# Performance work log

Hardware: AMD Instinct MI355X
Metric: run time of the kernel (lower is better)

## Reference

```python
import jax, jax.numpy as jnp
import numpy as np
import math

B, LQ, LK = 2, 2048, 2048
DIM = 1024
H = 16
DH = DIM // H


def setup_inputs() -> dict:
    key = jax.random.key(0)
    ks = jax.random.split(key, 12)
    s = 1.0 / math.sqrt(DIM)
    return {
        "query": jax.random.normal(ks[0], (B, LQ, DIM), jnp.float32),
        "key": jax.random.normal(ks[1], (B, LK, DIM), jnp.float32),
        "value": jax.random.normal(ks[2], (B, LK, DIM), jnp.float32),
        "mask": jnp.zeros((B, LQ, LK), dtype=bool),
        "Wq": jax.random.normal(ks[3], (DIM, DIM), jnp.float32) * s,
        "bq": jax.random.normal(ks[4], (DIM,), jnp.float32) * s,
        "Wk": jax.random.normal(ks[5], (DIM, DIM), jnp.float32) * s,
        "bk": jax.random.normal(ks[6], (DIM,), jnp.float32) * s,
        "Wv": jax.random.normal(ks[7], (DIM, DIM), jnp.float32) * s,
        "bv": jax.random.normal(ks[8], (DIM,), jnp.float32) * s,
        "Wo": jax.random.normal(ks[9], (DIM, DIM), jnp.float32) * s,
        "bo": jax.random.normal(ks[10], (DIM,), jnp.float32) * s,
    }


def reference(query, key, value, mask, Wq, bq, Wk, bk, Wv, bv, Wo, bo):
    b = query.shape[0]

    def shape(x):  # (b, l, dim) -> (b, h, l, dh)
        return x.reshape(b, -1, H, DH).transpose(0, 2, 1, 3)

    q = shape(query @ Wq.T + bq)
    k = shape(key @ Wk.T + bk)
    v = shape(value @ Wv.T + bv)

    q = q / math.sqrt(DH)
    # (b, h, lq, lk) score matrix, computed in float32 as the original does
    scores = jnp.einsum("bhqd,bhkd->bhqk", q, k).astype(jnp.float32)
    scores = jnp.where(mask[:, None, :, :], jnp.float32(-1e18), scores)
    attn = jax.nn.softmax(scores, axis=-1).astype(q.dtype)
    context = jnp.einsum("bhqk,bhkd->bhqd", attn, v)
    context = context.transpose(0, 2, 1, 3).reshape(b, -1, H * DH)
    return context @ Wo.T + bo
```

## Files before the change

kernel.cpp:

```cpp
#include <hip/hip_runtime.h>
#include <hip/hip_bf16.h>

typedef __attribute__((ext_vector_type(4))) float float4v;
typedef __attribute__((ext_vector_type(8))) __bf16 bf16x8;
typedef __attribute__((ext_vector_type(4))) unsigned short ushort4v;

#define MFMA16(a, b, c) __builtin_amdgcn_mfma_f32_16x16x32_bf16(a, b, c, 0, 0, 0)

__device__ __forceinline__ unsigned short f2bf(float f) {
    return __builtin_bit_cast(unsigned short, (__bf16)f);
}

__device__ __forceinline__ float fast_exp2(float x) {
#if __has_builtin(__builtin_amdgcn_exp2f)
    return __builtin_amdgcn_exp2f(x);
#else
    return exp2f(x);
#endif
}

__device__ __forceinline__ void gl_lds16(const unsigned short* g, unsigned short* l) {
    __builtin_amdgcn_global_load_lds(
        (const __attribute__((address_space(1))) void*)g,
        (__attribute__((address_space(3))) void*)l, 16, 0, 0);
}

struct CvtSeg { const float* s; unsigned short* d; int n; };
struct Cvt7 { CvtSeg seg[7]; };

__global__ __launch_bounds__(256) void cvt_kernel(Cvt7 a) {
    const CvtSeg c = a.seg[blockIdx.y];
    const int stride = gridDim.x * 256 * 4;
    for (int i = (blockIdx.x * 256 + threadIdx.x) * 4; i < c.n; i += stride) {
        float4v v = *(const float4v*)(c.s + i);
        ushort4v u;
        u.x = f2bf(v.x); u.y = f2bf(v.y); u.z = f2bf(v.z); u.w = f2bf(v.w);
        *(ushort4v*)(c.d + i) = u;
    }
}

__device__ __forceinline__ void gemm128_body(const unsigned short* __restrict__ A,
                                             const unsigned short* __restrict__ W,
                                             const float* __restrict__ bias,
                                             unsigned short* __restrict__ Cout,
                                             int N, int K, float scale,
                                             unsigned short* As, unsigned short* Ws) {
    const int t = threadIdx.x;
    const int w = t >> 6, lane = t & 63;
    const int quad = lane >> 4, l16 = lane & 15;
    const int m0 = blockIdx.x * 128, n0 = blockIdx.y * 128;
    const int wm = (w >> 1) * 64, wn = (w & 1) * 64;

    float4v acc[4][4];
    for (int i = 0; i < 4; ++i)
        for (int j = 0; j < 4; ++j) acc[i][j] = float4v{0.f, 0.f, 0.f, 0.f};

    const int srow = lane >> 3;
    const int scol = (lane & 7) * 8;

    for (int k0 = 0; k0 < K; k0 += 64) {
        __syncthreads();
        for (int i = 0; i < 4; ++i) {
            const int c = w * 4 + i;
            gl_lds16(A + (size_t)(m0 + c * 8 + srow) * K + k0 + scol,
                     &As[c * 512 + lane * 8]);
            gl_lds16(W + (size_t)(n0 + c * 8 + srow) * K + k0 + scol,
                     &Ws[c * 512 + lane * 8]);
        }
        __syncthreads();
        for (int ks = 0; ks < 2; ++ks) {
            bf16x8 af[4], wf[4];
            for (int i = 0; i < 4; ++i)
                af[i] = *(const bf16x8*)&As[(wm + i * 16 + l16) * 64 + ks * 32 + quad * 8];
            for (int i = 0; i < 4; ++i)
                wf[i] = *(const bf16x8*)&Ws[(wn + i * 16 + l16) * 64 + ks * 32 + quad * 8];
            for (int mi = 0; mi < 4; ++mi)
                for (int ni = 0; ni < 4; ++ni)
                    acc[mi][ni] = MFMA16(af[mi], wf[ni], acc[mi][ni]);
        }
    }

    for (int mi = 0; mi < 4; ++mi)
        for (int ni = 0; ni < 4; ++ni) {
            const int col = n0 + wn + ni * 16 + l16;
            const float bv = bias[col];
            for (int reg = 0; reg < 4; ++reg) {
                const int row = m0 + wm + mi * 16 + quad * 4 + reg;
                Cout[(size_t)row * N + col] = f2bf((acc[mi][ni][reg] + bv) * scale);
            }
        }
}

__global__ __launch_bounds__(256) void gemm_qkv_kernel(
    const unsigned short* qa, const unsigned short* ka, const unsigned short* va,
    const unsigned short* Wqb, const unsigned short* Wkb, const unsigned short* Wvb,
    const float* bq, const float* bk, const float* bv,
    unsigned short* Qb, unsigned short* Kb, unsigned short* Vb, float qscale) {
    __shared__ unsigned short As[128 * 64];
    __shared__ unsigned short Ws[128 * 64];
    const int z = blockIdx.z;
    const unsigned short* A = z == 0 ? qa : (z == 1 ? ka : va);
    const unsigned short* W = z == 0 ? Wqb : (z == 1 ? Wkb : Wvb);
    const float* bias = z == 0 ? bq : (z == 1 ? bk : bv);
    unsigned short* C = z == 0 ? Qb : (z == 1 ? Kb : Vb);
    gemm128_body(A, W, bias, C, 1024, 1024, z == 0 ? qscale : 1.0f, As, Ws);
}

__global__ __launch_bounds__(256) void gemm_out_kernel(const unsigned short* __restrict__ A,
                                                       const unsigned short* __restrict__ W,
                                                       const float* __restrict__ bias,
                                                       float* __restrict__ Cout) {
    __shared__ unsigned short As[64 * 64];
    __shared__ unsigned short Ws[128 * 64];
    const int N = 1024, K = 1024;
    const int t = threadIdx.x;
    const int w = t >> 6, lane = t & 63;
    const int quad = lane >> 4, l16 = lane & 15;
    const int m0 = blockIdx.x * 64, n0 = blockIdx.y * 128;
    const int wm = (w & 1) * 32, wn = (w >> 1) * 64;

    float4v acc[2][4];
    for (int i = 0; i < 2; ++i)
        for (int j = 0; j < 4; ++j) acc[i][j] = float4v{0.f, 0.f, 0.f, 0.f};

    const int srow = lane >> 3;
    const int scol = (lane & 7) * 8;

    for (int k0 = 0; k0 < K; k0 += 64) {
        __syncthreads();
        for (int i = 0; i < 2; ++i) {
            const int c = w * 2 + i;
            gl_lds16(A + (size_t)(m0 + c * 8 + srow) * K + k0 + scol,
                     &As[c * 512 + lane * 8]);
        }
        for (int i = 0; i < 4; ++i) {
            const int c = w * 4 + i;
            gl_lds16(W + (size_t)(n0 + c * 8 + srow) * K + k0 + scol,
                     &Ws[c * 512 + lane * 8]);
        }
        __syncthreads();
        for (int ks = 0; ks < 2; ++ks) {
            bf16x8 af[2], wf[4];
            for (int i = 0; i < 2; ++i)
                af[i] = *(const bf16x8*)&As[(wm + i * 16 + l16) * 64 + ks * 32 + quad * 8];
            for (int i = 0; i < 4; ++i)
                wf[i] = *(const bf16x8*)&Ws[(wn + i * 16 + l16) * 64 + ks * 32 + quad * 8];
            for (int mi = 0; mi < 2; ++mi)
                for (int ni = 0; ni < 4; ++ni)
                    acc[mi][ni] = MFMA16(af[mi], wf[ni], acc[mi][ni]);
        }
    }

    for (int mi = 0; mi < 2; ++mi)
        for (int ni = 0; ni < 4; ++ni) {
            const int col = n0 + wn + ni * 16 + l16;
            const float bv = bias[col];
            for (int reg = 0; reg < 4; ++reg) {
                const int row = m0 + wm + mi * 16 + quad * 4 + reg;
                Cout[(size_t)row * N + col] = acc[mi][ni][reg] + bv;
            }
        }
}

__global__ __launch_bounds__(256) void attn_kernel(const unsigned short* __restrict__ Q,
                                                   const unsigned short* __restrict__ Kg,
                                                   const unsigned short* __restrict__ Vg,
                                                   const unsigned char* __restrict__ mask,
                                                   unsigned short* __restrict__ Ctx) {
    const int bid = blockIdx.x;
    const int bh = bid & 31;
    const int qt = bid >> 5;
    const int b = bh >> 4, h = bh & 15;
    const int t = threadIdx.x, w = t >> 6, lane = t & 63;
    const int quad = lane >> 4, l16 = lane & 15;

    __shared__ unsigned short Pt[128][72];
    __shared__ unsigned short Ks[64][72];
    __shared__ unsigned short Vt[64][72];

    const unsigned short* Qp = Q + ((size_t)(b * 2048 + qt * 128)) * 1024 + h * 64;
    const unsigned short* Kp = Kg + ((size_t)b * 2048) * 1024 + h * 64;
    const unsigned short* Vp = Vg + ((size_t)b * 2048) * 1024 + h * 64;
    const unsigned char* Mp = mask + (size_t)(b * 2048 + qt * 128) * 2048;

    for (int p = 0; p < 4; ++p) {
        const int idx = t + p * 256;
        const int r = idx >> 3, c8 = (idx & 7) * 8;
        *(uint4*)&Pt[r][c8] = *(const uint4*)(Qp + (size_t)r * 1024 + c8);
    }
    __syncthreads();
    bf16x8 qf[2][2];
    for (int c = 0; c < 2; ++c)
        for (int ks = 0; ks < 2; ++ks)
            qf[c][ks] = *(const bf16x8*)&Pt[w * 32 + c * 16 + l16][ks * 32 + quad * 8];

    float4v o[2][4];
    for (int c = 0; c < 2; ++c)
        for (int i = 0; i < 4; ++i) o[c][i] = float4v{0.f, 0.f, 0.f, 0.f};
    float l_acc[2] = {0.f, 0.f};

    const int sr = t >> 3, sc8 = (t & 7) * 8;
    const int vkk = (t & 31) * 2, vd0 = (t >> 5) * 8;
    const int mrow = w * 32 + (lane >> 1);
    const int mc0 = (lane & 1) * 32;

    uint4 kreg0, kreg1, vreg0, vreg1, mreg0, mreg1;
    {
        kreg0 = *(const uint4*)(Kp + (size_t)sr * 1024 + sc8);
        kreg1 = *(const uint4*)(Kp + (size_t)(sr + 32) * 1024 + sc8);
        vreg0 = *(const uint4*)(Vp + (size_t)vkk * 1024 + vd0);
        vreg1 = *(const uint4*)(Vp + (size_t)(vkk + 1) * 1024 + vd0);
        mreg0 = *(const uint4*)(Mp + (size_t)mrow * 2048 + mc0);
        mreg1 = *(const uint4*)(Mp + (size_t)mrow * 2048 + mc0 + 16);
    }

    for (int kc = 0; kc < 2048; kc += 64) {
        __syncthreads();
        *(uint4*)&Ks[sr][sc8] = kreg0;
        *(uint4*)&Ks[sr + 32][sc8] = kreg1;
        {
            const unsigned short* pa = (const unsigned short*)&vreg0;
            const unsigned short* pb = (const unsigned short*)&vreg1;
            for (int j = 0; j < 8; ++j)
                *(unsigned int*)&Vt[vd0 + j][vkk] =
                    (unsigned int)pa[j] | ((unsigned int)pb[j] << 16);
        }
        const unsigned int mor = mreg0.x | mreg0.y | mreg0.z | mreg0.w |
                                 mreg1.x | mreg1.y | mreg1.z | mreg1.w;
        const bool anymask = __any(mor != 0);
        __syncthreads();

        const int kn = kc + 64;
        if (kn < 2048) {
            kreg0 = *(const uint4*)(Kp + (size_t)(kn + sr) * 1024 + sc8);
            kreg1 = *(const uint4*)(Kp + (size_t)(kn + sr + 32) * 1024 + sc8);
            vreg0 = *(const uint4*)(Vp + (size_t)(kn + vkk) * 1024 + vd0);
            vreg1 = *(const uint4*)(Vp + (size_t)(kn + vkk + 1) * 1024 + vd0);
            mreg0 = *(const uint4*)(Mp + (size_t)mrow * 2048 + kn + mc0);
            mreg1 = *(const uint4*)(Mp + (size_t)mrow * 2048 + kn + mc0 + 16);
        }

        float4v s0[4], s1[4];
        for (int nt = 0; nt < 4; ++nt) {
            const float4v z4 = float4v{0.f, 0.f, 0.f, 0.f};
            bf16x8 kf = *(const bf16x8*)&Ks[nt * 16 + l16][quad * 8];
            s0[nt] = MFMA16(kf, qf[0][0], z4);
            s1[nt] = MFMA16(kf, qf[1][0], z4);
            kf = *(const bf16x8*)&Ks[nt * 16 + l16][32 + quad * 8];
            s0[nt] = MFMA16(kf, qf[0][1], s0[nt]);
            s1[nt] = MFMA16(kf, qf[1][1], s1[nt]);
        }

        for (int c = 0; c < 2; ++c) {
            float4v* s = c ? s1 : s0;
            const int qrow = w * 32 + c * 16 + l16;
            float lc = l_acc[c];
            for (int nt = 0; nt < 4; ++nt) {
                float p0 = s[nt][0], p1 = s[nt][1], p2 = s[nt][2], p3 = s[nt][3];
                if (anymask) {
                    const unsigned char* mr =
                        Mp + (size_t)qrow * 2048 + kc + nt * 16 + quad * 4;
                    if (mr[0]) p0 = -1e18f;
                    if (mr[1]) p1 = -1e18f;
                    if (mr[2]) p2 = -1e18f;
                    if (mr[3]) p3 = -1e18f;
                }
                const float e0 = fast_exp2(p0), e1 = fast_exp2(p1);
                const float e2 = fast_exp2(p2), e3 = fast_exp2(p3);
                lc += (e0 + e1) + (e2 + e3);
                uint2 u;
                u.x = (unsigned int)f2bf(e0) | ((unsigned int)f2bf(e1) << 16);
                u.y = (unsigned int)f2bf(e2) | ((unsigned int)f2bf(e3) << 16);
                *(uint2*)&Pt[qrow][nt * 16 + quad * 4] = u;
            }
            l_acc[c] = lc;
        }

        for (int ks = 0; ks < 2; ++ks) {
            bf16x8 pf0 = *(const bf16x8*)&Pt[w * 32 + l16][ks * 32 + quad * 8];
            bf16x8 pf1 = *(const bf16x8*)&Pt[w * 32 + 16 + l16][ks * 32 + quad * 8];
            for (int dt = 0; dt < 4; ++dt) {
                bf16x8 vf = *(const bf16x8*)&Vt[dt * 16 + l16][ks * 32 + quad * 8];
                o[0][dt] = MFMA16(pf0, vf, o[0][dt]);
                o[1][dt] = MFMA16(pf1, vf, o[1][dt]);
            }
        }
    }

    float lfull[2];
    for (int c = 0; c < 2; ++c) {
        float l = l_acc[c];
        l += __shfl_xor(l, 16);
        l += __shfl_xor(l, 32);
        lfull[c] = l;
    }

    for (int c = 0; c < 2; ++c) {
        float inv[4];
        for (int reg = 0; reg < 4; ++reg)
            inv[reg] = 1.0f / __shfl(lfull[c], (lane & 48) | (quad * 4 + reg));
        for (int dt = 0; dt < 4; ++dt) {
            const int dcol = dt * 16 + l16;
            for (int reg = 0; reg < 4; ++reg) {
                const int ql = w * 32 + c * 16 + quad * 4 + reg;
                Ctx[((size_t)(b * 2048 + qt * 128 + ql)) * 1024 + h * 64 + dcol] =
                    f2bf(o[c][dt][reg] * inv[reg]);
            }
        }
    }
}

extern "C" void kernel_launch(void* const* d_in, const int* in_sizes, int n_in,
                              void* d_out, int out_size, void* d_ws, size_t ws_size,
                              hipStream_t stream) {
    (void)in_sizes; (void)n_in; (void)out_size; (void)ws_size;
    const float* query = (const float*)d_in[0];
    const float* key   = (const float*)d_in[1];
    const float* value = (const float*)d_in[2];
    const unsigned char* mask = (const unsigned char*)d_in[3];
    const float* Wq = (const float*)d_in[4];
    const float* bq = (const float*)d_in[5];
    const float* Wk = (const float*)d_in[6];
    const float* bk = (const float*)d_in[7];
    const float* Wv = (const float*)d_in[8];
    const float* bv = (const float*)d_in[9];
    const float* Wo = (const float*)d_in[10];
    const float* bo = (const float*)d_in[11];

    const size_t MD = (size_t)4096 * 1024;
    const size_t WD = (size_t)1024 * 1024;

    unsigned short* Qb  = (unsigned short*)d_ws;
    unsigned short* Kb  = Qb + MD;
    unsigned short* Vb  = Kb + MD;
    unsigned short* qb  = Vb + MD;
    unsigned short* kb  = qb + MD;
    unsigned short* vb  = kb + MD;
    unsigned short* Wqb = vb + MD;
    unsigned short* Wkb = Wqb + WD;
    unsigned short* Wvb = Wkb + WD;
    unsigned short* Wob = Wvb + WD;
    unsigned short* Cb  = qb;

    Cvt7 cv;
    cv.seg[0] = {query, qb, (int)MD};
    cv.seg[1] = {key,   kb, (int)MD};
    cv.seg[2] = {value, vb, (int)MD};
    cv.seg[3] = {Wq, Wqb, (int)WD};
    cv.seg[4] = {Wk, Wkb, (int)WD};
    cv.seg[5] = {Wv, Wvb, (int)WD};
    cv.seg[6] = {Wo, Wob, (int)WD};
    cvt_kernel<<<dim3(1024, 7), 256, 0, stream>>>(cv);

    const float qscale = 0.125f * 1.44269504088896f;
    gemm_qkv_kernel<<<dim3(32, 8, 3), 256, 0, stream>>>(
        qb, kb, vb, Wqb, Wkb, Wvb, bq, bk, bv, Qb, Kb, Vb, qscale);

    attn_kernel<<<dim3(512), 256, 0, stream>>>(Qb, Kb, Vb, mask, Cb);

    gemm_out_kernel<<<dim3(64, 8), 256, 0, stream>>>(Cb, Wob, bo, (float*)d_out);
}
```

Baseline: 268.0 us.

## Split attention over key dimension into two halves and merge partials

Splits the attention kernel along the key axis into two halves, launching 1024 blocks instead of 512. Each block writes unnormalized fp32 output and row-sum partials to workspace, and a merge kernel combines them and normalizes. This works without rescaling because the softmax uses no running max. The aim is better occupancy on the GPU's many CUs, at the cost of an extra kernel launch and the partial-buffer writes and reads. The old kernel remains as a fallback when the workspace is too small.

```diff
diff --git a/kernel.cpp b/kernel.cpp
--- a/kernel.cpp
+++ b/kernel.cpp
@@ -162,14 +162,16 @@
         }
 }
 
-__global__ __launch_bounds__(256) void attn_kernel(const unsigned short* __restrict__ Q,
-                                                   const unsigned short* __restrict__ Kg,
-                                                   const unsigned short* __restrict__ Vg,
-                                                   const unsigned char* __restrict__ mask,
-                                                   unsigned short* __restrict__ Ctx) {
+__global__ __launch_bounds__(256, 4) void attn_split_kernel(
+        const unsigned short* __restrict__ Q,
+        const unsigned short* __restrict__ Kg,
+        const unsigned short* __restrict__ Vg,
+        const unsigned char* __restrict__ mask,
+        float* __restrict__ Opart, float* __restrict__ Lpart) {
     const int bid = blockIdx.x;
     const int bh = bid & 31;
-    const int qt = bid >> 5;
+    const int qt = (bid >> 5) & 15;
+    const int half = bid >> 9;
     const int b = bh >> 4, h = bh & 15;
     const int t = threadIdx.x, w = t >> 6, lane = t & 63;
     const int quad = lane >> 4, l16 = lane & 15;
@@ -204,17 +206,20 @@
     const int mrow = w * 32 + (lane >> 1);
     const int mc0 = (lane & 1) * 32;
 
+    const int kbase = half << 10;
+    const int kend = kbase + 1024;
+
     uint4 kreg0, kreg1, vreg0, vreg1, mreg0, mreg1;
     {
-        kreg0 = *(const uint4*)(Kp + (size_t)sr * 1024 + sc8);
-        kreg1 = *(const uint4*)(Kp + (size_t)(sr + 32) * 1024 + sc8);
-        vreg0 = *(const uint4*)(Vp + (size_t)vkk * 1024 + vd0);
-        vreg1 = *(const uint4*)(Vp + (size_t)(vkk + 1) * 1024 + vd0);
-        mreg0 = *(const uint4*)(Mp + (size_t)mrow * 2048 + mc0);
-        mreg1 = *(const uint4*)(Mp + (size_t)mrow * 2048 + mc0 + 16);
-    }
-
-    for (int kc = 0; kc < 2048; kc += 64) {
+        kreg0 = *(const uint4*)(Kp + (size_t)(kbase + sr) * 1024 + sc8);
+        kreg1 = *(const uint4*)(Kp + (size_t)(kbase + sr + 32) * 1024 + sc8);
+        vreg0 = *(const uint4*)(Vp + (size_t)(kbase + vkk) * 1024 + vd0);
+        vreg1 = *(const uint4*)(Vp + (size_t)(kbase + vkk + 1) * 1024 + vd0);
+        mreg0 = *(const uint4*)(Mp + (size_t)mrow * 2048 + kbase + mc0);
+        mreg1 = *(const uint4*)(Mp + (size_t)mrow * 2048 + kbase + mc0 + 16);
+    }
+
+    for (int kc = kbase; kc < kend; kc += 64) {
         __syncthreads();
         *(uint4*)&Ks[sr][sc8] = kreg0;
         *(uint4*)&Ks[sr + 32][sc8] = kreg1;
@@ -231,7 +236,7 @@
         __syncthreads();
 
         const int kn = kc + 64;
-        if (kn < 2048) {
+        if (kn < kend) {
             kreg0 = *(const uint4*)(Kp + (size_t)(kn + sr) * 1024 + sc8);
             kreg1 = *(const uint4*)(Kp + (size_t)(kn + sr + 32) * 1024 + sc8);
             vreg0 = *(const uint4*)(Vp + (size_t)(kn + vkk) * 1024 + vd0);
@@ -295,6 +300,186 @@
         lfull[c] = l;
     }
 
+    const int pb = bid & 511;
+    float* Op = Opart + (size_t)half * (512 * 8192) + (size_t)pb * 8192;
+    float* Lp = Lpart + (size_t)half * (512 * 128) + (size_t)pb * 128;
+    for (int c = 0; c < 2; ++c) {
+        if (quad == 0) Lp[w * 32 + c * 16 + l16] = lfull[c];
+        for (int dt = 0; dt < 4; ++dt) {
+            const int dcol = dt * 16 + l16;
+            for (int reg = 0; reg < 4; ++reg) {
+                const int ql = w * 32 + c * 16 + quad * 4 + reg;
+                Op[ql * 64 + dcol] = o[c][dt][reg];
+            }
+        }
+    }
+}
+
+__global__ __launch_bounds__(256) void attn_merge_kernel(
+        const float* __restrict__ Opart, const float* __restrict__ Lpart,
+        unsigned short* __restrict__ Ctx) {
+    const int pb = blockIdx.x;
+    const int bh = pb & 31, qt = pb >> 5;
+    const int b = bh >> 4, h = bh & 15;
+    const int t = threadIdx.x;
+    __shared__ float invl[128];
+    if (t < 128) {
+        const float l0 = Lpart[(size_t)pb * 128 + t];
+        const float l1 = Lpart[(size_t)(512 * 128) + (size_t)pb * 128 + t];
+        invl[t] = 1.0f / (l0 + l1);
+    }
+    __syncthreads();
+    const float* O0 = Opart + (size_t)pb * 8192;
+    const float* O1 = Opart + (size_t)(512 * 8192) + (size_t)pb * 8192;
+    for (int i = 0; i < 8; ++i) {
+        const int idx4 = t + i * 256;
+        const int ql = idx4 >> 4;
+        const int d4 = (idx4 & 15) * 4;
+        const float4v a = *(const float4v*)(O0 + (size_t)idx4 * 4);
+        const float4v c = *(const float4v*)(O1 + (size_t)idx4 * 4);
+        const float s = invl[ql];
+        ushort4v u;
+        u.x = f2bf((a.x + c.x) * s);
+        u.y = f2bf((a.y + c.y) * s);
+        u.z = f2bf((a.z + c.z) * s);
+        u.w = f2bf((a.w + c.w) * s);
+        *(ushort4v*)(Ctx + ((size_t)(b * 2048 + qt * 128 + ql)) * 1024 + h * 64 + d4) = u;
+    }
+}
+
+__global__ __launch_bounds__(256) void attn_kernel(const unsigned short* __restrict__ Q,
+                                                   const unsigned short* __restrict__ Kg,
+                                                   const unsigned short* __restrict__ Vg,
+                                                   const unsigned char* __restrict__ mask,
+                                                   unsigned short* __restrict__ Ctx) {
+    const int bid = blockIdx.x;
+    const int bh = bid & 31;
+    const int qt = bid >> 5;
+    const int b = bh >> 4, h = bh & 15;
+    const int t = threadIdx.x, w = t >> 6, lane = t & 63;
+    const int quad = lane >> 4, l16 = lane & 15;
+
+    __shared__ unsigned short Pt[128][72];
+    __shared__ unsigned short Ks[64][72];
+    __shared__ unsigned short Vt[64][72];
+
+    const unsigned short* Qp = Q + ((size_t)(b * 2048 + qt * 128)) * 1024 + h * 64;
+    const unsigned short* Kp = Kg + ((size_t)b * 2048) * 1024 + h * 64;
+    const unsigned short* Vp = Vg + ((size_t)b * 2048) * 1024 + h * 64;
+    const unsigned char* Mp = mask + (size_t)(b * 2048 + qt * 128) * 2048;
+
+    for (int p = 0; p < 4; ++p) {
+        const int idx = t + p * 256;
+        const int r = idx >> 3, c8 = (idx & 7) * 8;
+        *(uint4*)&Pt[r][c8] = *(const uint4*)(Qp + (size_t)r * 1024 + c8);
+    }
+    __syncthreads();
+    bf16x8 qf[2][2];
+    for (int c = 0; c < 2; ++c)
+        for (int ks = 0; ks < 2; ++ks)
+            qf[c][ks] = *(const bf16x8*)&Pt[w * 32 + c * 16 + l16][ks * 32 + quad * 8];
+
+    float4v o[2][4];
+    for (int c = 0; c < 2; ++c)
+        for (int i = 0; i < 4; ++i) o[c][i] = float4v{0.f, 0.f, 0.f, 0.f};
+    float l_acc[2] = {0.f, 0.f};
+
+    const int sr = t >> 3, sc8 = (t & 7) * 8;
+    const int vkk = (t & 31) * 2, vd0 = (t >> 5) * 8;
+    const int mrow = w * 32 + (lane >> 1);
+    const int mc0 = (lane & 1) * 32;
+
+    uint4 kreg0, kreg1, vreg0, vreg1, mreg0, mreg1;
+    {
+        kreg0 = *(const uint4*)(Kp + (size_t)sr * 1024 + sc8);
+        kreg1 = *(const uint4*)(Kp + (size_t)(sr + 32) * 1024 + sc8);
+        vreg0 = *(const uint4*)(Vp + (size_t)vkk * 1024 + vd0);
+        vreg1 = *(const uint4*)(Vp + (size_t)(vkk + 1) * 1024 + vd0);
+        mreg0 = *(const uint4*)(Mp + (size_t)mrow * 2048 + mc0);
+        mreg1 = *(const uint4*)(Mp + (size_t)mrow * 2048 + mc0 + 16);
+    }
+
+    for (int kc = 0; kc < 2048; kc += 64) {
+        __syncthreads();
+        *(uint4*)&Ks[sr][sc8] = kreg0;
+        *(uint4*)&Ks[sr + 32][sc8] = kreg1;
+        {
+            const unsigned short* pa = (const unsigned short*)&vreg0;
+            const unsigned short* pb = (const unsigned short*)&vreg1;
+            for (int j = 0; j < 8; ++j)
+                *(unsigned int*)&Vt[vd0 + j][vkk] =
+                    (unsigned int)pa[j] | ((unsigned int)pb[j] << 16);
+        }
+        const unsigned int mor = mreg0.x | mreg0.y | mreg0.z | mreg0.w |
+                                 mreg1.x | mreg1.y | mreg1.z | mreg1.w;
+        const bool anymask = __any(mor != 0);
+        __syncthreads();
+
+        const int kn = kc + 64;
+        if (kn < 2048) {
+            kreg0 = *(const uint4*)(Kp + (size_t)(kn + sr) * 1024 + sc8);
+            kreg1 = *(const uint4*)(Kp + (size_t)(kn + sr + 32) * 1024 + sc8);
+            vreg0 = *(const uint4*)(Vp + (size_t)(kn + vkk) * 1024 + vd0);
+            vreg1 = *(const uint4*)(Vp + (size_t)(kn + vkk + 1) * 1024 + vd0);
+            mreg0 = *(const uint4*)(Mp + (size_t)mrow * 2048 + kn + mc0);
+            mreg1 = *(const uint4*)(Mp + (size_t)mrow * 2048 + kn + mc0 + 16);
+        }
+
+        float4v s0[4], s1[4];
+        for (int nt = 0; nt < 4; ++nt) {
+            const float4v z4 = float4v{0.f, 0.f, 0.f, 0.f};
+            bf16x8 kf = *(const bf16x8*)&Ks[nt * 16 + l16][quad * 8];
+            s0[nt] = MFMA16(kf, qf[0][0], z4);
+            s1[nt] = MFMA16(kf, qf[1][0], z4);
+            kf = *(const bf16x8*)&Ks[nt * 16 + l16][32 + quad * 8];
+            s0[nt] = MFMA16(kf, qf[0][1], s0[nt]);
+            s1[nt] = MFMA16(kf, qf[1][1], s1[nt]);
+        }
+
+        for (int c = 0; c < 2; ++c) {
+            float4v* s = c ? s1 : s0;
+            const int qrow = w * 32 + c * 16 + l16;
+            float lc = l_acc[c];
+            for (int nt = 0; nt < 4; ++nt) {
+                float p0 = s[nt][0], p1 = s[nt][1], p2 = s[nt][2], p3 = s[nt][3];
+                if (anymask) {
+                    const unsigned char* mr =
+                        Mp + (size_t)qrow * 2048 + kc + nt * 16 + quad * 4;
+                    if (mr[0]) p0 = -1e18f;
+                    if (mr[1]) p1 = -1e18f;
+                    if (mr[2]) p2 = -1e18f;
+                    if (mr[3]) p3 = -1e18f;
+                }
+                const float e0 = fast_exp2(p0), e1 = fast_exp2(p1);
+                const float e2 = fast_exp2(p2), e3 = fast_exp2(p3);
+                lc += (e0 + e1) + (e2 + e3);
+                uint2 u;
+                u.x = (unsigned int)f2bf(e0) | ((unsigned int)f2bf(e1) << 16);
+                u.y = (unsigned int)f2bf(e2) | ((unsigned int)f2bf(e3) << 16);
+                *(uint2*)&Pt[qrow][nt * 16 + quad * 4] = u;
+            }
+            l_acc[c] = lc;
+        }
+
+        for (int ks = 0; ks < 2; ++ks) {
+            bf16x8 pf0 = *(const bf16x8*)&Pt[w * 32 + l16][ks * 32 + quad * 8];
+            bf16x8 pf1 = *(const bf16x8*)&Pt[w * 32 + 16 + l16][ks * 32 + quad * 8];
+            for (int dt = 0; dt < 4; ++dt) {
+                bf16x8 vf = *(const bf16x8*)&Vt[dt * 16 + l16][ks * 32 + quad * 8];
+                o[0][dt] = MFMA16(pf0, vf, o[0][dt]);
+                o[1][dt] = MFMA16(pf1, vf, o[1][dt]);
+            }
+        }
+    }
+
+    float lfull[2];
+    for (int c = 0; c < 2; ++c) {
+        float l = l_acc[c];
+        l += __shfl_xor(l, 16);
+        l += __shfl_xor(l, 32);
+        lfull[c] = l;
+    }
+
     for (int c = 0; c < 2; ++c) {
         float inv[4];
         for (int reg = 0; reg < 4; ++reg)
@@ -313,7 +498,7 @@
 extern "C" void kernel_launch(void* const* d_in, const int* in_sizes, int n_in,
                               void* d_out, int out_size, void* d_ws, size_t ws_size,
                               hipStream_t stream) {
-    (void)in_sizes; (void)n_in; (void)out_size; (void)ws_size;
+    (void)in_sizes; (void)n_in; (void)out_size;
     const float* query = (const float*)d_in[0];
     const float* key   = (const float*)d_in[1];
     const float* value = (const float*)d_in[2];
@@ -342,6 +527,11 @@
     unsigned short* Wob = Wvb + WD;
     unsigned short* Cb  = qb;
 
+    float* Opart = (float*)(Wob + WD);
+    float* Lpart = Opart + (size_t)2 * 512 * 8192;
+    const size_t need = (size_t)(6 * MD + 4 * WD) * 2 +
+                        ((size_t)2 * 512 * 8192 + (size_t)2 * 512 * 128) * 4;
+
     Cvt7 cv;
     cv.seg[0] = {query, qb, (int)MD};
     cv.seg[1] = {key,   kb, (int)MD};
@@ -356,7 +546,12 @@
     gemm_qkv_kernel<<<dim3(32, 8, 3), 256, 0, stream>>>(
         qb, kb, vb, Wqb, Wkb, Wvb, bq, bk, bv, Qb, Kb, Vb, qscale);
 
-    attn_kernel<<<dim3(512), 256, 0, stream>>>(Qb, Kb, Vb, mask, Cb);
+    if (ws_size >= need) {
+        attn_split_kernel<<<dim3(1024), 256, 0, stream>>>(Qb, Kb, Vb, mask, Opart, Lpart);
+        attn_merge_kernel<<<dim3(512), 256, 0, stream>>>(Opart, Lpart, Cb);
+    } else {
+        attn_kernel<<<dim3(512), 256, 0, stream>>>(Qb, Kb, Vb, mask, Cb);
+    }
 
     gemm_out_kernel<<<dim3(64, 8), 256, 0, stream>>>(Cb, Wob, bo, (float*)d_out);
 }
```

Measured after the change: 278.6 us. 1.04x slower.

## Remap GEMM block order per XCD, shrink out-proj tiles, widen cvt vectors

Applied to the files above, without the earlier changes.

The QKV and output GEMMs now use a flat 1D grid. Block ids are remapped with an (id&7)*stride+(id>>3) pattern so that consecutive work items land on the same XCD, which should improve L2 reuse of A/W tiles. The output projection tile shrinks from 64x128 to 64x64, doubling the block count to 1024 to improve occupancy and load balance, at the cost of less operand reuse per block. The conversion kernel now handles 8 elements per thread with 16-byte stores and uses half as many blocks.

```diff
diff --git a/kernel.cpp b/kernel.cpp
--- a/kernel.cpp
+++ b/kernel.cpp
@@ -4,6 +4,7 @@
 typedef __attribute__((ext_vector_type(4))) float float4v;
 typedef __attribute__((ext_vector_type(8))) __bf16 bf16x8;
 typedef __attribute__((ext_vector_type(4))) unsigned short ushort4v;
+typedef __attribute__((ext_vector_type(8))) unsigned short ushort8v;
 
 #define MFMA16(a, b, c) __builtin_amdgcn_mfma_f32_16x16x32_bf16(a, b, c, 0, 0, 0)
 
@@ -30,12 +31,14 @@
 
 __global__ __launch_bounds__(256) void cvt_kernel(Cvt7 a) {
     const CvtSeg c = a.seg[blockIdx.y];
-    const int stride = gridDim.x * 256 * 4;
-    for (int i = (blockIdx.x * 256 + threadIdx.x) * 4; i < c.n; i += stride) {
-        float4v v = *(const float4v*)(c.s + i);
-        ushort4v u;
-        u.x = f2bf(v.x); u.y = f2bf(v.y); u.z = f2bf(v.z); u.w = f2bf(v.w);
-        *(ushort4v*)(c.d + i) = u;
+    const int stride = gridDim.x * 256 * 8;
+    for (int i = (blockIdx.x * 256 + threadIdx.x) * 8; i < c.n; i += stride) {
+        float4v v0 = *(const float4v*)(c.s + i);
+        float4v v1 = *(const float4v*)(c.s + i + 4);
+        ushort8v u;
+        u[0] = f2bf(v0.x); u[1] = f2bf(v0.y); u[2] = f2bf(v0.z); u[3] = f2bf(v0.w);
+        u[4] = f2bf(v1.x); u[5] = f2bf(v1.y); u[6] = f2bf(v1.z); u[7] = f2bf(v1.w);
+        *(ushort8v*)(c.d + i) = u;
     }
 }
 
@@ -44,11 +47,11 @@
                                              const float* __restrict__ bias,
                                              unsigned short* __restrict__ Cout,
                                              int N, int K, float scale,
-                                             unsigned short* As, unsigned short* Ws) {
+                                             unsigned short* As, unsigned short* Ws,
+                                             int m0, int n0) {
     const int t = threadIdx.x;
     const int w = t >> 6, lane = t & 63;
     const int quad = lane >> 4, l16 = lane & 15;
-    const int m0 = blockIdx.x * 128, n0 = blockIdx.y * 128;
     const int wm = (w >> 1) * 64, wn = (w & 1) * 64;
 
     float4v acc[4][4];
@@ -98,12 +101,18 @@
     unsigned short* Qb, unsigned short* Kb, unsigned short* Vb, float qscale) {
     __shared__ unsigned short As[128 * 64];
     __shared__ unsigned short Ws[128 * 64];
-    const int z = blockIdx.z;
+    const int id = blockIdx.x;
+    const int work = (id & 7) * 96 + (id >> 3);
+    const int x = work & 31;
+    const int combo = work >> 5;
+    const int y = combo & 7;
+    const int z = combo >> 3;
     const unsigned short* A = z == 0 ? qa : (z == 1 ? ka : va);
     const unsigned short* W = z == 0 ? Wqb : (z == 1 ? Wkb : Wvb);
     const float* bias = z == 0 ? bq : (z == 1 ? bk : bv);
     unsigned short* C = z == 0 ? Qb : (z == 1 ? Kb : Vb);
-    gemm128_body(A, W, bias, C, 1024, 1024, z == 0 ? qscale : 1.0f, As, Ws);
+    gemm128_body(A, W, bias, C, 1024, 1024, z == 0 ? qscale : 1.0f, As, Ws,
+                 x * 128, y * 128);
 }
 
 __global__ __launch_bounds__(256) void gemm_out_kernel(const unsigned short* __restrict__ A,
@@ -111,17 +120,20 @@
                                                        const float* __restrict__ bias,
                                                        float* __restrict__ Cout) {
     __shared__ unsigned short As[64 * 64];
-    __shared__ unsigned short Ws[128 * 64];
+    __shared__ unsigned short Ws[64 * 64];
     const int N = 1024, K = 1024;
     const int t = threadIdx.x;
     const int w = t >> 6, lane = t & 63;
     const int quad = lane >> 4, l16 = lane & 15;
-    const int m0 = blockIdx.x * 64, n0 = blockIdx.y * 128;
-    const int wm = (w & 1) * 32, wn = (w >> 1) * 64;
-
-    float4v acc[2][4];
+    const int id = blockIdx.x;
+    const int work = (id & 7) * 128 + (id >> 3);
+    const int m0 = (work & 63) * 64;
+    const int n0 = (work >> 6) * 64;
+    const int wm = (w >> 1) * 32, wn = (w & 1) * 32;
+
+    float4v acc[2][2];
     for (int i = 0; i < 2; ++i)
-        for (int j = 0; j < 4; ++j) acc[i][j] = float4v{0.f, 0.f, 0.f, 0.f};
+        for (int j = 0; j < 2; ++j) acc[i][j] = float4v{0.f, 0.f, 0.f, 0.f};
 
     const int srow = lane >> 3;
     const int scol = (lane & 7) * 8;
@@ -132,27 +144,24 @@
             const int c = w * 2 + i;
             gl_lds16(A + (size_t)(m0 + c * 8 + srow) * K + k0 + scol,
                      &As[c * 512 + lane * 8]);
-        }
-        for (int i = 0; i < 4; ++i) {
-            const int c = w * 4 + i;
             gl_lds16(W + (size_t)(n0 + c * 8 + srow) * K + k0 + scol,
                      &Ws[c * 512 + lane * 8]);
         }
         __syncthreads();
         for (int ks = 0; ks < 2; ++ks) {
-            bf16x8 af[2], wf[4];
+            bf16x8 af[2], wf[2];
             for (int i = 0; i < 2; ++i)
                 af[i] = *(const bf16x8*)&As[(wm + i * 16 + l16) * 64 + ks * 32 + quad * 8];
-            for (int i = 0; i < 4; ++i)
+            for (int i = 0; i < 2; ++i)
                 wf[i] = *(const bf16x8*)&Ws[(wn + i * 16 + l16) * 64 + ks * 32 + quad * 8];
             for (int mi = 0; mi < 2; ++mi)
-                for (int ni = 0; ni < 4; ++ni)
+                for (int ni = 0; ni < 2; ++ni)
                     acc[mi][ni] = MFMA16(af[mi], wf[ni], acc[mi][ni]);
         }
     }
 
     for (int mi = 0; mi < 2; ++mi)
-        for (int ni = 0; ni < 4; ++ni) {
+        for (int ni = 0; ni < 2; ++ni) {
             const int col = n0 + wn + ni * 16 + l16;
             const float bv = bias[col];
             for (int reg = 0; reg < 4; ++reg) {
@@ -350,13 +359,13 @@
     cv.seg[4] = {Wk, Wkb, (int)WD};
     cv.seg[5] = {Wv, Wvb, (int)WD};
     cv.seg[6] = {Wo, Wob, (int)WD};
-    cvt_kernel<<<dim3(1024, 7), 256, 0, stream>>>(cv);
+    cvt_kernel<<<dim3(512, 7), 256, 0, stream>>>(cv);
 
     const float qscale = 0.125f * 1.44269504088896f;
-    gemm_qkv_kernel<<<dim3(32, 8, 3), 256, 0, stream>>>(
+    gemm_qkv_kernel<<<dim3(768), 256, 0, stream>>>(
         qb, kb, vb, Wqb, Wkb, Wvb, bq, bk, bv, Qb, Kb, Vb, qscale);
 
     attn_kernel<<<dim3(512), 256, 0, stream>>>(Qb, Kb, Vb, mask, Cb);
 
-    gemm_out_kernel<<<dim3(64, 8), 256, 0, stream>>>(Cb, Wob, bo, (float*)d_out);
-}
+    gemm_out_kernel<<<dim3(1024), 256, 0, stream>>>(Cb, Wob, bo, (float*)d_out);
+}
```

New measurement: 274.9 us. 1.03x slower.

## Fuse activation fp32-to-bf16 conversion into QKV GEMM and remap blocks

Applied to the files above, without the earlier changes.

Drops the standalone conversion of query/key/value to bf16. The QKV GEMM now loads fp32 activations straight into registers, converts them, and writes bf16 into LDS, which removes a full write and read of the converted activation buffers. The GEMM grid is flattened to 1D with a swizzled block-to-tile mapping meant to improve cache locality. The attention softmax/PV loop is also interleaved per k-slice, and the weight conversion kernel is widened to 8 elements per thread. In exchange, activation loads go through registers rather than direct-to-LDS loads, and the QKV GEMM reads twice as many bytes per A tile.

```diff
diff --git a/kernel.cpp b/kernel.cpp
--- a/kernel.cpp
+++ b/kernel.cpp
@@ -4,6 +4,7 @@
 typedef __attribute__((ext_vector_type(4))) float float4v;
 typedef __attribute__((ext_vector_type(8))) __bf16 bf16x8;
 typedef __attribute__((ext_vector_type(4))) unsigned short ushort4v;
+typedef __attribute__((ext_vector_type(8))) unsigned short ushort8v;
 
 #define MFMA16(a, b, c) __builtin_amdgcn_mfma_f32_16x16x32_bf16(a, b, c, 0, 0, 0)
 
@@ -26,29 +27,45 @@
 }
 
 struct CvtSeg { const float* s; unsigned short* d; int n; };
-struct Cvt7 { CvtSeg seg[7]; };
-
-__global__ __launch_bounds__(256) void cvt_kernel(Cvt7 a) {
+struct Cvt4 { CvtSeg seg[4]; };
+
+__global__ __launch_bounds__(256) void cvt_kernel(Cvt4 a) {
     const CvtSeg c = a.seg[blockIdx.y];
-    const int stride = gridDim.x * 256 * 4;
-    for (int i = (blockIdx.x * 256 + threadIdx.x) * 4; i < c.n; i += stride) {
-        float4v v = *(const float4v*)(c.s + i);
-        ushort4v u;
-        u.x = f2bf(v.x); u.y = f2bf(v.y); u.z = f2bf(v.z); u.w = f2bf(v.w);
-        *(ushort4v*)(c.d + i) = u;
-    }
-}
-
-__device__ __forceinline__ void gemm128_body(const unsigned short* __restrict__ A,
-                                             const unsigned short* __restrict__ W,
-                                             const float* __restrict__ bias,
-                                             unsigned short* __restrict__ Cout,
-                                             int N, int K, float scale,
-                                             unsigned short* As, unsigned short* Ws) {
+    const int stride = gridDim.x * 256 * 8;
+    for (int i = (blockIdx.x * 256 + threadIdx.x) * 8; i < c.n; i += stride) {
+        float4v v0 = *(const float4v*)(c.s + i);
+        float4v v1 = *(const float4v*)(c.s + i + 4);
+        ushort8v u;
+        u[0] = f2bf(v0.x); u[1] = f2bf(v0.y); u[2] = f2bf(v0.z); u[3] = f2bf(v0.w);
+        u[4] = f2bf(v1.x); u[5] = f2bf(v1.y); u[6] = f2bf(v1.z); u[7] = f2bf(v1.w);
+        *(ushort8v*)(c.d + i) = u;
+    }
+}
+
+__global__ __launch_bounds__(256) void gemm_qkv_kernel(
+    const float* qa, const float* ka, const float* va,
+    const unsigned short* Wqb, const unsigned short* Wkb, const unsigned short* Wvb,
+    const float* bq, const float* bk, const float* bv,
+    unsigned short* Qb, unsigned short* Kb, unsigned short* Vb, float qscale) {
+    __shared__ unsigned short As[128 * 64];
+    __shared__ unsigned short Ws[128 * 64];
+    const int id = blockIdx.x;
+    const int work = (id & 7) * 96 + (id >> 3);
+    const int x = work & 31;
+    const int combo = work >> 5;
+    const int y = combo & 7;
+    const int z = combo >> 3;
+    const float* A = z == 0 ? qa : (z == 1 ? ka : va);
+    const unsigned short* W = z == 0 ? Wqb : (z == 1 ? Wkb : Wvb);
+    const float* bias = z == 0 ? bq : (z == 1 ? bk : bv);
+    unsigned short* Cout = z == 0 ? Qb : (z == 1 ? Kb : Vb);
+    const float scale = z == 0 ? qscale : 1.0f;
+    const int m0 = x * 128, n0 = y * 128;
+    const int N = 1024, K = 1024;
+
     const int t = threadIdx.x;
     const int w = t >> 6, lane = t & 63;
     const int quad = lane >> 4, l16 = lane & 15;
-    const int m0 = blockIdx.x * 128, n0 = blockIdx.y * 128;
     const int wm = (w >> 1) * 64, wn = (w & 1) * 64;
 
     float4v acc[4][4];
@@ -59,11 +76,22 @@
     const int scol = (lane & 7) * 8;
 
     for (int k0 = 0; k0 < K; k0 += 64) {
-        __syncthreads();
+        float4v fa[4][2];
         for (int i = 0; i < 4; ++i) {
             const int c = w * 4 + i;
-            gl_lds16(A + (size_t)(m0 + c * 8 + srow) * K + k0 + scol,
-                     &As[c * 512 + lane * 8]);
+            const float* src = A + (size_t)(m0 + c * 8 + srow) * K + k0 + scol;
+            fa[i][0] = *(const float4v*)src;
+            fa[i][1] = *(const float4v*)(src + 4);
+        }
+        __syncthreads();
+        for (int i = 0; i < 4; ++i) {
+            const int c = w * 4 + i;
+            ushort8v u;
+            u[0] = f2bf(fa[i][0].x); u[1] = f2bf(fa[i][0].y);
+            u[2] = f2bf(fa[i][0].z); u[3] = f2bf(fa[i][0].w);
+            u[4] = f2bf(fa[i][1].x); u[5] = f2bf(fa[i][1].y);
+            u[6] = f2bf(fa[i][1].z); u[7] = f2bf(fa[i][1].w);
+            *(ushort8v*)&As[c * 512 + lane * 8] = u;
             gl_lds16(W + (size_t)(n0 + c * 8 + srow) * K + k0 + scol,
                      &Ws[c * 512 + lane * 8]);
         }
@@ -89,21 +117,6 @@
                 Cout[(size_t)row * N + col] = f2bf((acc[mi][ni][reg] + bv) * scale);
             }
         }
-}
-
-__global__ __launch_bounds__(256) void gemm_qkv_kernel(
-    const unsigned short* qa, const unsigned short* ka, const unsigned short* va,
-    const unsigned short* Wqb, const unsigned short* Wkb, const unsigned short* Wvb,
-    const float* bq, const float* bk, const float* bv,
-    unsigned short* Qb, unsigned short* Kb, unsigned short* Vb, float qscale) {
-    __shared__ unsigned short As[128 * 64];
-    __shared__ unsigned short Ws[128 * 64];
-    const int z = blockIdx.z;
-    const unsigned short* A = z == 0 ? qa : (z == 1 ? ka : va);
-    const unsigned short* W = z == 0 ? Wqb : (z == 1 ? Wkb : Wvb);
-    const float* bias = z == 0 ? bq : (z == 1 ? bk : bv);
-    unsigned short* C = z == 0 ? Qb : (z == 1 ? Kb : Vb);
-    gemm128_body(A, W, bias, C, 1024, 1024, z == 0 ? qscale : 1.0f, As, Ws);
 }
 
 __global__ __launch_bounds__(256) void gemm_out_kernel(const unsigned short* __restrict__ A,
@@ -251,32 +264,31 @@
             s1[nt] = MFMA16(kf, qf[1][1], s1[nt]);
         }
 
-        for (int c = 0; c < 2; ++c) {
-            float4v* s = c ? s1 : s0;
-            const int qrow = w * 32 + c * 16 + l16;
-            float lc = l_acc[c];
-            for (int nt = 0; nt < 4; ++nt) {
-                float p0 = s[nt][0], p1 = s[nt][1], p2 = s[nt][2], p3 = s[nt][3];
-                if (anymask) {
-                    const unsigned char* mr =
-                        Mp + (size_t)qrow * 2048 + kc + nt * 16 + quad * 4;
-                    if (mr[0]) p0 = -1e18f;
-                    if (mr[1]) p1 = -1e18f;
-                    if (mr[2]) p2 = -1e18f;
-                    if (mr[3]) p3 = -1e18f;
+        for (int ks = 0; ks < 2; ++ks) {
+            for (int c = 0; c < 2; ++c) {
+                float4v* s = c ? s1 : s0;
+                const int qrow = w * 32 + c * 16 + l16;
+                float lc = l_acc[c];
+                for (int nt = ks * 2; nt < ks * 2 + 2; ++nt) {
+                    float p0 = s[nt][0], p1 = s[nt][1], p2 = s[nt][2], p3 = s[nt][3];
+                    if (anymask) {
+                        const unsigned char* mr =
+                            Mp + (size_t)qrow * 2048 + kc + nt * 16 + quad * 4;
+                        if (mr[0]) p0 = -1e18f;
+                        if (mr[1]) p1 = -1e18f;
+                        if (mr[2]) p2 = -1e18f;
+                        if (mr[3]) p3 = -1e18f;
+                    }
+                    const float e0 = fast_exp2(p0), e1 = fast_exp2(p1);
+                    const float e2 = fast_exp2(p2), e3 = fast_exp2(p3);
+                    lc += (e0 + e1) + (e2 + e3);
+                    uint2 u;
+                    u.x = (unsigned int)f2bf(e0) | ((unsigned int)f2bf(e1) << 16);
+                    u.y = (unsigned int)f2bf(e2) | ((unsigned int)f2bf(e3) << 16);
+                    *(uint2*)&Pt[qrow][nt * 16 + quad * 4] = u;
                 }
-                const float e0 = fast_exp2(p0), e1 = fast_exp2(p1);
-                const float e2 = fast_exp2(p2), e3 = fast_exp2(p3);
-                lc += (e0 + e1) + (e2 + e3);
-                uint2 u;
-                u.x = (unsigned int)f2bf(e0) | ((unsigned int)f2bf(e1) << 16);
-                u.y = (unsigned int)f2bf(e2) | ((unsigned int)f2bf(e3) << 16);
-                *(uint2*)&Pt[qrow][nt * 16 + quad * 4] = u;
-            }
-            l_acc[c] = lc;
-        }
-
-        for (int ks = 0; ks < 2; ++ks) {
+                l_acc[c] = lc;
+            }
             bf16x8 pf0 = *(const bf16x8*)&Pt[w * 32 + l16][ks * 32 + quad * 8];
             bf16x8 pf1 = *(const bf16x8*)&Pt[w * 32 + 16 + l16][ks * 32 + quad * 8];
             for (int dt = 0; dt < 4; ++dt) {
@@ -333,28 +345,22 @@
     unsigned short* Qb  = (unsigned short*)d_ws;
     unsigned short* Kb  = Qb + MD;
     unsigned short* Vb  = Kb + MD;
-    unsigned short* qb  = Vb + MD;
-    unsigned short* kb  = qb + MD;
-    unsigned short* vb  = kb + MD;
-    unsigned short* Wqb = vb + MD;
+    unsigned short* Wqb = Vb + MD;
     unsigned short* Wkb = Wqb + WD;
     unsigned short* Wvb = Wkb + WD;
     unsigned short* Wob = Wvb + WD;
-    unsigned short* Cb  = qb;
-
-    Cvt7 cv;
-    cv.seg[0] = {query, qb, (int)MD};
-    cv.seg[1] = {key,   kb, (int)MD};
-    cv.seg[2] = {value, vb, (int)MD};
-    cv.seg[3] = {Wq, Wqb, (int)WD};
-    cv.seg[4] = {Wk, Wkb, (int)WD};
-    cv.seg[5] = {Wv, Wvb, (int)WD};
-    cv.seg[6] = {Wo, Wob, (int)WD};
-    cvt_kernel<<<dim3(1024, 7), 256, 0, stream>>>(cv);
+    unsigned short* Cb  = Wob + WD;
+
+    Cvt4 cv;
+    cv.seg[0] = {Wq, Wqb, (int)WD};
+    cv.seg[1] = {Wk, Wkb, (int)WD};
+    cv.seg[2] = {Wv, Wvb, (int)WD};
+    cv.seg[3] = {Wo, Wob, (int)WD};
+    cvt_kernel<<<dim3(512, 4), 256, 0, stream>>>(cv);
 
     const float qscale = 0.125f * 1.44269504088896f;
-    gemm_qkv_kernel<<<dim3(32, 8, 3), 256, 0, stream>>>(
-        qb, kb, vb, Wqb, Wkb, Wvb, bq, bk, bv, Qb, Kb, Vb, qscale);
+    gemm_qkv_kernel<<<dim3(768), 256, 0, stream>>>(
+        query, key, value, Wqb, Wkb, Wvb, bq, bk, bv, Qb, Kb, Vb, qscale);
 
     attn_kernel<<<dim3(512), 256, 0, stream>>>(Qb, Kb, Vb, mask, Cb);
 
```

After: 275.3 us. 2.7% more time.
